# Kernel optimization log

Measured on AMD Instinct MI355X. Metric: run time of the kernel, lower is better.

The kernel has to match this reference:

```python
import jax, jax.numpy as jnp
import numpy as np
import math

B, H, S, D = 2, 16, 2048, 64

def setup_inputs() -> dict:
    key = jax.random.key(0)
    kq, kk, kv, km = jax.random.split(key, 4)
    return {
        "query": jax.random.normal(kq, (B, H, S, D), dtype=jnp.float32),
        "key": jax.random.normal(kk, (B, H, S, D), dtype=jnp.float32),
        "value": jax.random.normal(kv, (B, H, S, D), dtype=jnp.float32),
        "attn_mask": jax.random.normal(km, (B, 1, S, S), dtype=jnp.float32),
    }

def reference(query, key, value, attn_mask):
    # qk = Q K^T / sqrt(D)  -> [B,H,S,S]
    scale = 1.0 / math.sqrt(query.shape[-1])
    qk = jnp.einsum("bhqd,bhkd->bhqk", query, key) * scale
    qk = qk + attn_mask  # additive mask, broadcasts over heads
    attn_weight = jax.nn.softmax(qk, axis=-1)
    # dropout_p = 0.0 (undefined global in source; p=0 train-mode dropout is identity)
    output = jnp.einsum("bhqk,bhkd->bhqd", attn_weight, value)
    return output
```

## Files before the change

kernel.cpp:

```cpp
#include <hip/hip_runtime.h>

#define B_ 2
#define H_ 16
#define S_ 2048
#define D_ 64

typedef __attribute__((ext_vector_type(8))) _Float16 half8;
typedef __attribute__((ext_vector_type(2))) __fp16 fp16x2;
typedef __attribute__((ext_vector_type(16))) float f32x16;

constexpr int QW  = 32;
constexpr int NW  = 4;
constexpr int QB  = QW * NW;
constexpr int KVB = 32;
constexpr int NIT = S_ / KVB;

#define GLOBAL_AS(p) ((const __attribute__((address_space(1))) void*)(p))
#define LDS_AS(p)    ((__attribute__((address_space(3))) void*)(p))

__global__ __launch_bounds__(256)
void presplit(const float* __restrict__ Kg, const float* __restrict__ Vg,
              _Float16* __restrict__ W)
{
    const int t   = blockIdx.x;
    const int bh  = blockIdx.y;
    const int tid = threadIdx.x;

    const float* Kp = Kg + (size_t)bh * S_ * D_ + (size_t)t * KVB * D_;
    const float* Vp = Vg + (size_t)bh * S_ * D_ + (size_t)t * KVB * D_;
    _Float16*    Wp = W + ((size_t)bh * NIT + t) * 8192;

    {
        const int r = tid >> 3, l = tid & 7;
        const float* src = Kp + r * D_ + l * 8;
        float4 a = *(const float4*)src;
        float4 c = *(const float4*)(src + 4);
        float e[8] = {a.x, a.y, a.z, a.w, c.x, c.y, c.z, c.w};
        half8 hh, hl;
        #pragma unroll
        for (int j = 0; j < 8; ++j) {
            _Float16 h = (_Float16)e[j];
            hh[j] = h;
            hl[j] = (_Float16)(e[j] - (float)h);
        }
        const int cs = l ^ (r & 7);
        *(half8*)&Wp[r * 64 + cs * 8]        = hh;
        *(half8*)&Wp[2048 + r * 64 + cs * 8] = hl;
    }
    {
        const int d = tid & 63, c = tid >> 6;
        float e[8];
        #pragma unroll
        for (int j = 0; j < 8; ++j) e[j] = Vp[(size_t)(c * 8 + j) * D_ + d];
        half8 hh, hl;
        #pragma unroll
        for (int j = 0; j < 8; ++j) {
            _Float16 h = (_Float16)e[j];
            hh[j] = h;
            hl[j] = (_Float16)(e[j] - (float)h);
        }
        const int cw = c ^ (d & 3) ^ ((d >> 2) & 3);
        *(half8*)&Wp[4096 + d * 32 + cw * 8] = hh;
        *(half8*)&Wp[6144 + d * 32 + cw * 8] = hl;
    }
}

__global__ __launch_bounds__(256, 2)
void fattn2(const float* __restrict__ Qg, const float* __restrict__ Mg,
            const _Float16* __restrict__ W, float* __restrict__ Og)
{
    const int tid  = threadIdx.x;
    const int lane = tid & 63;
    const int lo32 = tid & 31;
    const int hi   = (tid >> 5) & 1;
    const int wv   = tid >> 6;

    const int qblk = blockIdx.x;
    const int bh   = blockIdx.y;
    const int b    = bh >> 4;

    const float* Qp = Qg + (size_t)bh * S_ * D_;
    const float* Mp = Mg + (size_t)b  * S_ * S_;
    float*       Op = Og + (size_t)bh * S_ * D_;
    const _Float16* Wp = W + (size_t)bh * NIT * 8192;

    __shared__ __align__(16) _Float16 TILE[2][8192];

    const int qloc = qblk * QB + wv * QW + lo32;

    half8 Qhi[4], Qlo[4];
    #pragma unroll
    for (int f = 0; f < 4; ++f) {
        const float* src = Qp + (size_t)qloc * D_ + f * 16 + hi * 8;
        float4 a = *(const float4*)src;
        float4 c = *(const float4*)(src + 4);
        float v8[8] = {a.x, a.y, a.z, a.w, c.x, c.y, c.z, c.w};
        half8 hh, hl;
        #pragma unroll
        for (int j = 0; j < 8; ++j) {
            _Float16 h = (_Float16)v8[j];
            hh[j] = h;
            hl[j] = (_Float16)(v8[j] - (float)h);
        }
        Qhi[f] = hh; Qlo[f] = hl;
    }

    f32x16 acc0, acc1;
    #pragma unroll
    for (int i = 0; i < 16; ++i) { acc0[i] = 0.f; acc1[i] = 0.f; }
    float mrun = -1e30f, lrun = 0.f;

    const float kScL2 = 0.125f * 1.44269504088896340736f;
    const float kL2E  = 1.44269504088896340736f;

    float4 mcur[4], mnxt[4];

    auto stage = [&](int bf, int t) {
        const _Float16* src = Wp + (size_t)t * 8192 + wv * 2048 + lane * 8;
        _Float16* dst = &TILE[bf][wv * 2048];
        #pragma unroll
        for (int c = 0; c < 4; ++c)
            __builtin_amdgcn_global_load_lds(GLOBAL_AS(src + c * 512),
                                             LDS_AS(dst + c * 512), 16, 0, 0);
    };
    auto mask_load = [&](int kv, float4* mv) {
        const float* mrow = Mp + (size_t)qloc * S_ + kv;
        #pragma unroll
        for (int g = 0; g < 4; ++g) mv[g] = *(const float4*)(mrow + 8 * g + 4 * hi);
    };

    stage(0, 0);
    mask_load(0, mcur);
    __syncthreads();

    for (int t = 0; t < NIT; ++t) {
        const int bf = t & 1;
        if (t + 1 < NIT) {
            mask_load((t + 1) * KVB, mnxt);
            stage(bf ^ 1, t + 1);
        }

        f32x16 s;
        #pragma unroll
        for (int i = 0; i < 16; ++i) s[i] = 0.f;
        __builtin_amdgcn_s_setprio(1);
        #pragma unroll
        for (int f = 0; f < 4; ++f) {
            const int cs = (2 * f + hi) ^ (lo32 & 7);
            half8 ah = *(const half8*)&TILE[bf][lo32 * 64 + cs * 8];
            half8 al = *(const half8*)&TILE[bf][2048 + lo32 * 64 + cs * 8];
            s = __builtin_amdgcn_mfma_f32_32x32x16_f16(ah, Qhi[f], s, 0, 0, 0);
            s = __builtin_amdgcn_mfma_f32_32x32x16_f16(al, Qhi[f], s, 0, 0, 0);
            s = __builtin_amdgcn_mfma_f32_32x32x16_f16(ah, Qlo[f], s, 0, 0, 0);
        }
        __builtin_amdgcn_s_setprio(0);

        float p[16];
        #pragma unroll
        for (int g = 0; g < 4; ++g) {
            p[4*g+0] = fmaf(s[4*g+0], kScL2, mcur[g].x * kL2E);
            p[4*g+1] = fmaf(s[4*g+1], kScL2, mcur[g].y * kL2E);
            p[4*g+2] = fmaf(s[4*g+2], kScL2, mcur[g].z * kL2E);
            p[4*g+3] = fmaf(s[4*g+3], kScL2, mcur[g].w * kL2E);
        }

        float mt = p[0];
        #pragma unroll
        for (int r = 1; r < 16; ++r) mt = fmaxf(mt, p[r]);
        mt = fmaxf(mt, __shfl_xor(mt, 32));
        if (!__all(mt - mrun <= 8.0f)) {
            const float mnew = fmaxf(mrun, mt);
            const float corr = __builtin_amdgcn_exp2f(mrun - mnew);
            lrun *= corr;
            #pragma unroll
            for (int i = 0; i < 16; ++i) { acc0[i] *= corr; acc1[i] *= corr; }
            mrun = mnew;
        }
        float ps = 0.f;
        #pragma unroll
        for (int r = 0; r < 16; ++r) {
            p[r] = __builtin_amdgcn_exp2f(p[r] - mrun);
            ps += p[r];
        }
        ps += __shfl_xor(ps, 32);
        lrun += ps;

        int dw[8], px[8];
        #pragma unroll
        for (int g = 0; g < 4; ++g) {
            union { fp16x2 h; int i; } u0, u1;
            u0.h = __builtin_amdgcn_cvt_pkrtz(p[4*g+0], p[4*g+1]);
            u1.h = __builtin_amdgcn_cvt_pkrtz(p[4*g+2], p[4*g+3]);
            dw[2*g]   = u0.i;
            dw[2*g+1] = u1.i;
        }
        #pragma unroll
        for (int i = 0; i < 8; ++i) px[i] = __shfl_xor(dw[i], 32);

        half8 Pf[2];
        #pragma unroll
        for (int ks = 0; ks < 2; ++ks) {
            union { int i[4]; half8 h; } f;
            f.i[0] = hi ? px[4*ks+2] : dw[4*ks+0];
            f.i[1] = hi ? px[4*ks+3] : dw[4*ks+1];
            f.i[2] = hi ? dw[4*ks+2] : px[4*ks+0];
            f.i[3] = hi ? dw[4*ks+3] : px[4*ks+1];
            Pf[ks] = f.h;
        }

        __builtin_amdgcn_s_setprio(1);
        #pragma unroll
        for (int ks = 0; ks < 2; ++ks) {
            const int c0 = (2 * ks + hi) ^ (lo32 & 3) ^ ((lo32 >> 2) & 3);
            half8 vh0 = *(const half8*)&TILE[bf][4096 + lo32        * 32 + c0 * 8];
            half8 vl0 = *(const half8*)&TILE[bf][6144 + lo32        * 32 + c0 * 8];
            half8 vh1 = *(const half8*)&TILE[bf][4096 + (32 + lo32) * 32 + c0 * 8];
            half8 vl1 = *(const half8*)&TILE[bf][6144 + (32 + lo32) * 32 + c0 * 8];
            acc0 = __builtin_amdgcn_mfma_f32_32x32x16_f16(vh0, Pf[ks], acc0, 0, 0, 0);
            acc0 = __builtin_amdgcn_mfma_f32_32x32x16_f16(vl0, Pf[ks], acc0, 0, 0, 0);
            acc1 = __builtin_amdgcn_mfma_f32_32x32x16_f16(vh1, Pf[ks], acc1, 0, 0, 0);
            acc1 = __builtin_amdgcn_mfma_f32_32x32x16_f16(vl1, Pf[ks], acc1, 0, 0, 0);
        }
        __builtin_amdgcn_s_setprio(0);

        #pragma unroll
        for (int g = 0; g < 4; ++g) mcur[g] = mnxt[g];
        __syncthreads();
    }

    const float inv = 1.0f / lrun;
    #pragma unroll
    for (int r = 0; r < 16; ++r) {
        const int drow = (r & 3) + 8 * (r >> 2) + 4 * hi;
        Op[(size_t)qloc * D_ + drow]      = acc0[r] * inv;
        Op[(size_t)qloc * D_ + 32 + drow] = acc1[r] * inv;
    }
}

__global__ __launch_bounds__(128, 2)
void fattn(const float* __restrict__ Qg, const float* __restrict__ Kg,
           const float* __restrict__ Vg, const float* __restrict__ Mg,
           float* __restrict__ Og)
{
    const int tid  = threadIdx.x;
    const int lo32 = tid & 31;
    const int hi   = (tid >> 5) & 1;
    const int wv   = tid >> 6;

    const int qblk = blockIdx.x;
    const int bh   = blockIdx.y;
    const int b    = bh >> 4;

    const float* Qp = Qg + (size_t)bh * S_ * D_;
    const float* Kp = Kg + (size_t)bh * S_ * D_;
    const float* Vp = Vg + (size_t)bh * S_ * D_;
    const float* Mp = Mg + (size_t)b  * S_ * S_;
    float*       Op = Og + (size_t)bh * S_ * D_;

    __shared__ __align__(16) _Float16 Khi[2][KVB * D_];
    __shared__ __align__(16) _Float16 Klo[2][KVB * D_];
    __shared__ __align__(16) _Float16 VThi[2][D_ * KVB];
    __shared__ __align__(16) _Float16 VTlo[2][D_ * KVB];

    const int qloc = qblk * 64 + wv * QW + lo32;

    const int ksr = tid >> 2;
    const int ksc = tid & 3;
    const int vd  = tid & 63;
    const int vw  = tid >> 6;

    half8 Qhi[4], Qlo[4];
    #pragma unroll
    for (int f = 0; f < 4; ++f) {
        const float* src = Qp + (size_t)qloc * D_ + f * 16 + hi * 8;
        float4 a = *(const float4*)src;
        float4 c = *(const float4*)(src + 4);
        float v8[8] = {a.x, a.y, a.z, a.w, c.x, c.y, c.z, c.w};
        half8 hh, hl;
        #pragma unroll
        for (int j = 0; j < 8; ++j) {
            _Float16 h = (_Float16)v8[j];
            hh[j] = h;
            hl[j] = (_Float16)(v8[j] - (float)h);
        }
        Qhi[f] = hh; Qlo[f] = hl;
    }

    f32x16 acc0, acc1;
    #pragma unroll
    for (int i = 0; i < 16; ++i) { acc0[i] = 0.f; acc1[i] = 0.f; }
    float mrun = -1e30f, lrun = 0.f;

    const float kScL2 = 0.125f * 1.44269504088896340736f;
    const float kL2E  = 1.44269504088896340736f;

    float4 kr[4];
    float  vr[16];
    float4 mcur[4], mnxt[4];

    auto stage_load = [&](int kv) {
        const float* ks = Kp + (size_t)(kv + ksr) * D_ + ksc * 16;
        #pragma unroll
        for (int i = 0; i < 4; ++i) kr[i] = *(const float4*)(ks + 4 * i);
        const float* vs = Vp + (size_t)(kv + vw * 16) * D_ + vd;
        #pragma unroll
        for (int r = 0; r < 16; ++r) vr[r] = vs[(size_t)r * D_];
    };
    auto stage_write = [&](int bf) {
        #pragma unroll
        for (int u = 0; u < 2; ++u) {
            float e[8] = {kr[2*u].x, kr[2*u].y, kr[2*u].z, kr[2*u].w,
                          kr[2*u+1].x, kr[2*u+1].y, kr[2*u+1].z, kr[2*u+1].w};
            half8 hh, hl;
            #pragma unroll
            for (int j = 0; j < 8; ++j) {
                _Float16 h = (_Float16)e[j];
                hh[j] = h;
                hl[j] = (_Float16)(e[j] - (float)h);
            }
            const int cs = (ksc * 2 + u) ^ (ksr & 7);
            *(half8*)&Khi[bf][ksr * 64 + cs * 8] = hh;
            *(half8*)&Klo[bf][ksr * 64 + cs * 8] = hl;
        }
        #pragma unroll
        for (int u = 0; u < 2; ++u) {
            half8 hh, hl;
            #pragma unroll
            for (int j = 0; j < 8; ++j) {
                float x = vr[8*u + j];
                _Float16 h = (_Float16)x;
                hh[j] = h;
                hl[j] = (_Float16)(x - (float)h);
            }
            const int c = (vw * 2 + u) ^ (vd & 3) ^ ((vd >> 2) & 3);
            *(half8*)&VThi[bf][vd * 32 + c * 8] = hh;
            *(half8*)&VTlo[bf][vd * 32 + c * 8] = hl;
        }
    };
    auto mask_load = [&](int kv, float4* mv) {
        const float* mrow = Mp + (size_t)qloc * S_ + kv;
        #pragma unroll
        for (int g = 0; g < 4; ++g) mv[g] = *(const float4*)(mrow + 8 * g + 4 * hi);
    };

    stage_load(0);
    stage_write(0);
    mask_load(0, mcur);
    __syncthreads();

    for (int t = 0; t < NIT; ++t) {
        const int bf = t & 1;
        if (t + 1 < NIT) {
            mask_load((t + 1) * KVB, mnxt);
            stage_load((t + 1) * KVB);
        }

        f32x16 s;
        #pragma unroll
        for (int i = 0; i < 16; ++i) s[i] = 0.f;
        #pragma unroll
        for (int f = 0; f < 4; ++f) {
            const int cs = (2 * f + hi) ^ (lo32 & 7);
            half8 ah = *(const half8*)&Khi[bf][lo32 * 64 + cs * 8];
            half8 al = *(const half8*)&Klo[bf][lo32 * 64 + cs * 8];
            s = __builtin_amdgcn_mfma_f32_32x32x16_f16(ah, Qhi[f], s, 0, 0, 0);
            s = __builtin_amdgcn_mfma_f32_32x32x16_f16(al, Qhi[f], s, 0, 0, 0);
            s = __builtin_amdgcn_mfma_f32_32x32x16_f16(ah, Qlo[f], s, 0, 0, 0);
        }

        float p[16];
        #pragma unroll
        for (int g = 0; g < 4; ++g) {
            p[4*g+0] = fmaf(s[4*g+0], kScL2, mcur[g].x * kL2E);
            p[4*g+1] = fmaf(s[4*g+1], kScL2, mcur[g].y * kL2E);
            p[4*g+2] = fmaf(s[4*g+2], kScL2, mcur[g].z * kL2E);
            p[4*g+3] = fmaf(s[4*g+3], kScL2, mcur[g].w * kL2E);
        }

        float mt = p[0];
        #pragma unroll
        for (int r = 1; r < 16; ++r) mt = fmaxf(mt, p[r]);
        mt = fmaxf(mt, __shfl_xor(mt, 32));
        const float mnew = fmaxf(mrun, mt);
        const float corr = __builtin_amdgcn_exp2f(mrun - mnew);
        float ps = 0.f;
        #pragma unroll
        for (int r = 0; r < 16; ++r) {
            p[r] = __builtin_amdgcn_exp2f(p[r] - mnew);
            ps += p[r];
        }
        ps += __shfl_xor(ps, 32);
        lrun = lrun * corr + ps;
        mrun = mnew;
        #pragma unroll
        for (int i = 0; i < 16; ++i) { acc0[i] *= corr; acc1[i] *= corr; }

        int dw[8], px[8];
        #pragma unroll
        for (int g = 0; g < 4; ++g) {
            union { fp16x2 h; int i; } u0, u1;
            u0.h = __builtin_amdgcn_cvt_pkrtz(p[4*g+0], p[4*g+1]);
            u1.h = __builtin_amdgcn_cvt_pkrtz(p[4*g+2], p[4*g+3]);
            dw[2*g]   = u0.i;
            dw[2*g+1] = u1.i;
        }
        #pragma unroll
        for (int i = 0; i < 8; ++i) px[i] = __shfl_xor(dw[i], 32);

        half8 Pf[2];
        #pragma unroll
        for (int ks = 0; ks < 2; ++ks) {
            union { int i[4]; half8 h; } f;
            f.i[0] = hi ? px[4*ks+2] : dw[4*ks+0];
            f.i[1] = hi ? px[4*ks+3] : dw[4*ks+1];
            f.i[2] = hi ? dw[4*ks+2] : px[4*ks+0];
            f.i[3] = hi ? dw[4*ks+3] : px[4*ks+1];
            Pf[ks] = f.h;
        }

        #pragma unroll
        for (int ks = 0; ks < 2; ++ks) {
            const int c0 = (2 * ks + hi) ^ (lo32 & 3) ^ ((lo32 >> 2) & 3);
            half8 vh0 = *(const half8*)&VThi[bf][lo32        * 32 + c0 * 8];
            half8 vl0 = *(const half8*)&VTlo[bf][lo32        * 32 + c0 * 8];
            half8 vh1 = *(const half8*)&VThi[bf][(32 + lo32) * 32 + c0 * 8];
            half8 vl1 = *(const half8*)&VTlo[bf][(32 + lo32) * 32 + c0 * 8];
            acc0 = __builtin_amdgcn_mfma_f32_32x32x16_f16(vh0, Pf[ks], acc0, 0, 0, 0);
            acc0 = __builtin_amdgcn_mfma_f32_32x32x16_f16(vl0, Pf[ks], acc0, 0, 0, 0);
            acc1 = __builtin_amdgcn_mfma_f32_32x32x16_f16(vh1, Pf[ks], acc1, 0, 0, 0);
            acc1 = __builtin_amdgcn_mfma_f32_32x32x16_f16(vl1, Pf[ks], acc1, 0, 0, 0);
        }

        if (t + 1 < NIT) stage_write(bf ^ 1);
        #pragma unroll
        for (int g = 0; g < 4; ++g) mcur[g] = mnxt[g];
        __syncthreads();
    }

    const float inv = 1.0f / lrun;
    #pragma unroll
    for (int r = 0; r < 16; ++r) {
        const int drow = (r & 3) + 8 * (r >> 2) + 4 * hi;
        Op[(size_t)qloc * D_ + drow]      = acc0[r] * inv;
        Op[(size_t)qloc * D_ + 32 + drow] = acc1[r] * inv;
    }
}

extern "C" void kernel_launch(void* const* d_in, const int* in_sizes, int n_in,
                              void* d_out, int out_size, void* d_ws, size_t ws_size,
                              hipStream_t stream)
{
    (void)in_sizes; (void)n_in; (void)out_size;
    const float* Q = (const float*)d_in[0];
    const float* K = (const float*)d_in[1];
    const float* V = (const float*)d_in[2];
    const float* M = (const float*)d_in[3];
    float* O = (float*)d_out;

    const size_t need = (size_t)(B_ * H_) * NIT * 8192 * sizeof(_Float16);
    if (ws_size >= need) {
        _Float16* W = (_Float16*)d_ws;
        presplit<<<dim3(NIT, B_ * H_), 256, 0, stream>>>(K, V, W);
        fattn2<<<dim3(S_ / QB, B_ * H_), 256, 0, stream>>>(Q, M, W, O);
    } else {
        fattn<<<dim3(S_ / 64, B_ * H_), 128, 0, stream>>>(Q, K, V, M, O);
    }
}
```

Before: 223.3 us.

## Split KV range across two blocks and combine partial softmax results

Adds a split-KV variant of the attention kernel that processes half of the key/value tiles per block and writes unnormalized partial outputs plus running max/sum to workspace. A new combine kernel merges the two halves using log-sum-exp rescaling. The aim is to double the grid (from 512 to 1024 blocks) for better CU occupancy on the GPU, and launch bounds rise to 4 blocks per CU. The cost is an extra kernel launch and extra global traffic for the partial outputs, plus register pressure from the tighter launch bound.

```diff
diff --git a/kernel.cpp b/kernel.cpp
--- a/kernel.cpp
+++ b/kernel.cpp
@@ -14,6 +14,8 @@
 constexpr int QB  = QW * NW;
 constexpr int KVB = 32;
 constexpr int NIT = S_ / KVB;
+constexpr int SPL = 2;
+constexpr int NITS = NIT / SPL;
 
 #define GLOBAL_AS(p) ((const __attribute__((address_space(1))) void*)(p))
 #define LDS_AS(p)    ((__attribute__((address_space(3))) void*)(p))
@@ -63,6 +65,200 @@
         *(half8*)&Wp[4096 + d * 32 + cw * 8] = hh;
         *(half8*)&Wp[6144 + d * 32 + cw * 8] = hl;
     }
+}
+
+__global__ __launch_bounds__(256, 4)
+void fattn2s(const float* __restrict__ Qg, const float* __restrict__ Mg,
+             const _Float16* __restrict__ W, float* __restrict__ Opart,
+             float2* __restrict__ ML)
+{
+    const int tid  = threadIdx.x;
+    const int lane = tid & 63;
+    const int lo32 = tid & 31;
+    const int hi   = (tid >> 5) & 1;
+    const int wv   = tid >> 6;
+
+    const int qblk = blockIdx.x;
+    const int bh   = blockIdx.y;
+    const int sp   = blockIdx.z;
+    const int b    = bh >> 4;
+    const int tb   = sp * NITS;
+
+    const float* Qp = Qg + (size_t)bh * S_ * D_;
+    const float* Mp = Mg + (size_t)b  * S_ * S_;
+    const _Float16* Wp = W + (size_t)bh * NIT * 8192;
+
+    __shared__ __align__(16) _Float16 TILE[2][8192];
+
+    const int qloc = qblk * QB + wv * QW + lo32;
+
+    half8 Qhi[4], Qlo[4];
+    #pragma unroll
+    for (int f = 0; f < 4; ++f) {
+        const float* src = Qp + (size_t)qloc * D_ + f * 16 + hi * 8;
+        float4 a = *(const float4*)src;
+        float4 c = *(const float4*)(src + 4);
+        float v8[8] = {a.x, a.y, a.z, a.w, c.x, c.y, c.z, c.w};
+        half8 hh, hl;
+        #pragma unroll
+        for (int j = 0; j < 8; ++j) {
+            _Float16 h = (_Float16)v8[j];
+            hh[j] = h;
+            hl[j] = (_Float16)(v8[j] - (float)h);
+        }
+        Qhi[f] = hh; Qlo[f] = hl;
+    }
+
+    f32x16 acc0, acc1;
+    #pragma unroll
+    for (int i = 0; i < 16; ++i) { acc0[i] = 0.f; acc1[i] = 0.f; }
+    float mrun = -1e30f, lrun = 0.f;
+
+    const float kScL2 = 0.125f * 1.44269504088896340736f;
+    const float kL2E  = 1.44269504088896340736f;
+
+    float4 mcur[4], mnxt[4];
+
+    auto stage = [&](int bf, int tg) {
+        const _Float16* src = Wp + (size_t)tg * 8192 + wv * 2048 + lane * 8;
+        _Float16* dst = &TILE[bf][wv * 2048];
+        #pragma unroll
+        for (int c = 0; c < 4; ++c)
+            __builtin_amdgcn_global_load_lds(GLOBAL_AS(src + c * 512),
+                                             LDS_AS(dst + c * 512), 16, 0, 0);
+    };
+    auto mask_load = [&](int kv, float4* mv) {
+        const float* mrow = Mp + (size_t)qloc * S_ + kv;
+        #pragma unroll
+        for (int g = 0; g < 4; ++g) mv[g] = *(const float4*)(mrow + 8 * g + 4 * hi);
+    };
+
+    stage(0, tb);
+    mask_load(tb * KVB, mcur);
+    __syncthreads();
+
+    for (int t = 0; t < NITS; ++t) {
+        const int bf = t & 1;
+        if (t + 1 < NITS) {
+            mask_load((tb + t + 1) * KVB, mnxt);
+            stage(bf ^ 1, tb + t + 1);
+        }
+
+        f32x16 s;
+        #pragma unroll
+        for (int i = 0; i < 16; ++i) s[i] = 0.f;
+        __builtin_amdgcn_s_setprio(1);
+        #pragma unroll
+        for (int f = 0; f < 4; ++f) {
+            const int cs = (2 * f + hi) ^ (lo32 & 7);
+            half8 ah = *(const half8*)&TILE[bf][lo32 * 64 + cs * 8];
+            half8 al = *(const half8*)&TILE[bf][2048 + lo32 * 64 + cs * 8];
+            s = __builtin_amdgcn_mfma_f32_32x32x16_f16(ah, Qhi[f], s, 0, 0, 0);
+            s = __builtin_amdgcn_mfma_f32_32x32x16_f16(al, Qhi[f], s, 0, 0, 0);
+            s = __builtin_amdgcn_mfma_f32_32x32x16_f16(ah, Qlo[f], s, 0, 0, 0);
+        }
+        __builtin_amdgcn_s_setprio(0);
+
+        float p[16];
+        #pragma unroll
+        for (int g = 0; g < 4; ++g) {
+            p[4*g+0] = fmaf(s[4*g+0], kScL2, mcur[g].x * kL2E);
+            p[4*g+1] = fmaf(s[4*g+1], kScL2, mcur[g].y * kL2E);
+            p[4*g+2] = fmaf(s[4*g+2], kScL2, mcur[g].z * kL2E);
+            p[4*g+3] = fmaf(s[4*g+3], kScL2, mcur[g].w * kL2E);
+        }
+
+        float mt = p[0];
+        #pragma unroll
+        for (int r = 1; r < 16; ++r) mt = fmaxf(mt, p[r]);
+        mt = fmaxf(mt, __shfl_xor(mt, 32));
+        if (!__all(mt - mrun <= 8.0f)) {
+            const float mnew = fmaxf(mrun, mt);
+            const float corr = __builtin_amdgcn_exp2f(mrun - mnew);
+            lrun *= corr;
+            #pragma unroll
+            for (int i = 0; i < 16; ++i) { acc0[i] *= corr; acc1[i] *= corr; }
+            mrun = mnew;
+        }
+        float ps = 0.f;
+        #pragma unroll
+        for (int r = 0; r < 16; ++r) {
+            p[r] = __builtin_amdgcn_exp2f(p[r] - mrun);
+            ps += p[r];
+        }
+        ps += __shfl_xor(ps, 32);
+        lrun += ps;
+
+        int dw[8], px[8];
+        #pragma unroll
+        for (int g = 0; g < 4; ++g) {
+            union { fp16x2 h; int i; } u0, u1;
+            u0.h = __builtin_amdgcn_cvt_pkrtz(p[4*g+0], p[4*g+1]);
+            u1.h = __builtin_amdgcn_cvt_pkrtz(p[4*g+2], p[4*g+3]);
+            dw[2*g]   = u0.i;
+            dw[2*g+1] = u1.i;
+        }
+        #pragma unroll
+        for (int i = 0; i < 8; ++i) px[i] = __shfl_xor(dw[i], 32);
+
+        half8 Pf[2];
+        #pragma unroll
+        for (int ks = 0; ks < 2; ++ks) {
+            union { int i[4]; half8 h; } f;
+            f.i[0] = hi ? px[4*ks+2] : dw[4*ks+0];
+            f.i[1] = hi ? px[4*ks+3] : dw[4*ks+1];
+            f.i[2] = hi ? dw[4*ks+2] : px[4*ks+0];
+            f.i[3] = hi ? dw[4*ks+3] : px[4*ks+1];
+            Pf[ks] = f.h;
+        }
+
+        __builtin_amdgcn_s_setprio(1);
+        #pragma unroll
+        for (int ks = 0; ks < 2; ++ks) {
+            const int c0 = (2 * ks + hi) ^ (lo32 & 3) ^ ((lo32 >> 2) & 3);
+            half8 vh0 = *(const half8*)&TILE[bf][4096 + lo32        * 32 + c0 * 8];
+            half8 vl0 = *(const half8*)&TILE[bf][6144 + lo32        * 32 + c0 * 8];
+            half8 vh1 = *(const half8*)&TILE[bf][4096 + (32 + lo32) * 32 + c0 * 8];
+            half8 vl1 = *(const half8*)&TILE[bf][6144 + (32 + lo32) * 32 + c0 * 8];
+            acc0 = __builtin_amdgcn_mfma_f32_32x32x16_f16(vh0, Pf[ks], acc0, 0, 0, 0);
+            acc0 = __builtin_amdgcn_mfma_f32_32x32x16_f16(vl0, Pf[ks], acc0, 0, 0, 0);
+            acc1 = __builtin_amdgcn_mfma_f32_32x32x16_f16(vh1, Pf[ks], acc1, 0, 0, 0);
+            acc1 = __builtin_amdgcn_mfma_f32_32x32x16_f16(vl1, Pf[ks], acc1, 0, 0, 0);
+        }
+        __builtin_amdgcn_s_setprio(0);
+
+        #pragma unroll
+        for (int g = 0; g < 4; ++g) mcur[g] = mnxt[g];
+        __syncthreads();
+    }
+
+    const size_t r0 = ((size_t)sp * (B_ * H_) + bh) * S_ + qloc;
+    float* Po = Opart + r0 * D_;
+    #pragma unroll
+    for (int r = 0; r < 16; ++r) {
+        const int drow = (r & 3) + 8 * (r >> 2) + 4 * hi;
+        Po[drow]      = acc0[r];
+        Po[32 + drow] = acc1[r];
+    }
+    if (hi == 0) ML[r0] = make_float2(mrun, lrun);
+}
+
+__global__ __launch_bounds__(256)
+void combine(const float* __restrict__ Opart, const float2* __restrict__ ML,
+             float* __restrict__ O)
+{
+    const size_t NR = (size_t)B_ * H_ * S_;
+    const size_t r  = (size_t)blockIdx.x * 4 + (threadIdx.x >> 6);
+    const int lane  = threadIdx.x & 63;
+
+    const float2 a = ML[r];
+    const float2 c = ML[NR + r];
+    const float m  = fmaxf(a.x, c.x);
+    const float w1 = __builtin_amdgcn_exp2f(a.x - m);
+    const float w2 = __builtin_amdgcn_exp2f(c.x - m);
+    const float inv = 1.0f / (a.y * w1 + c.y * w2);
+    O[r * D_ + lane] = (Opart[r * D_ + lane] * w1 +
+                        Opart[NR * D_ + r * D_ + lane] * w2) * inv;
 }
 
 __global__ __launch_bounds__(256, 2)
@@ -457,8 +653,19 @@
     const float* M = (const float*)d_in[3];
     float* O = (float*)d_out;
 
-    const size_t need = (size_t)(B_ * H_) * NIT * 8192 * sizeof(_Float16);
-    if (ws_size >= need) {
+    const size_t NR     = (size_t)B_ * H_ * S_;
+    const size_t wBytes = (size_t)(B_ * H_) * NIT * 8192 * 2;
+    const size_t oBytes = (size_t)SPL * NR * D_ * 4;
+    const size_t mBytes = (size_t)SPL * NR * 8;
+
+    if (ws_size >= wBytes + oBytes + mBytes) {
+        _Float16* W  = (_Float16*)d_ws;
+        float*    Op = (float*)((char*)d_ws + wBytes);
+        float2*   ML = (float2*)((char*)d_ws + wBytes + oBytes);
+        presplit<<<dim3(NIT, B_ * H_), 256, 0, stream>>>(K, V, W);
+        fattn2s<<<dim3(S_ / QB, B_ * H_, SPL), 256, 0, stream>>>(Q, M, W, Op, ML);
+        combine<<<dim3(NR / 4), 256, 0, stream>>>(Op, ML, O);
+    } else if (ws_size >= wBytes) {
         _Float16* W = (_Float16*)d_ws;
         presplit<<<dim3(NIT, B_ * H_), 256, 0, stream>>>(K, V, W);
         fattn2<<<dim3(S_ / QB, B_ * H_), 256, 0, stream>>>(Q, M, W, O);
```

Result: slower. 294.1 us (+31.7%).
